# Optimization experiments

Measured on AMD Instinct MI355X. Metric: run time of the kernel, lower is better.

## Reference

```python
import jax, jax.numpy as jnp
import numpy as np
import math

B, S, H = 8, 1024, 768
NH = 12
DH = H // NH


def _linear(x, W, b):
    # torch Linear: y = x @ W.T + b, W: [out, in]
    return jnp.einsum('bsd,ed->bse', x, W) + b


def _split_heads(x):
    # [B,S,H] -> [B,NH,S,DH]
    b, s, _ = x.shape
    return x.reshape(b, s, NH, DH).transpose(0, 2, 1, 3)


def _attend(q, k, v):
    # q,k,v: [B,NH,S,DH]
    scores = jnp.einsum('bhqd,bhkd->bhqk', q, k) / math.sqrt(DH)
    probs = jax.nn.softmax(scores, axis=-1)
    ctx = jnp.einsum('bhqk,bhkd->bhqd', probs, v)
    b, h, s, d = ctx.shape
    return ctx.transpose(0, 2, 1, 3).reshape(b, s, h * d)


def setup_inputs() -> dict:
    key = jax.random.key(0)
    ks = jax.random.split(key, 20)
    sc = 1.0 / math.sqrt(H)
    inp = {
        'hidden_statesx': jax.random.normal(ks[0], (B, S, H), jnp.float32),
        'hidden_statesy': jax.random.normal(ks[1], (B, S, H), jnp.float32),
    }
    names = ['Wq', 'Wk', 'Wv', 'Wo', 'Wqd', 'Wkd', 'Wvd', 'Wod']
    for i, n in enumerate(names):
        inp[n] = jax.random.normal(ks[2 + i], (H, H), jnp.float32) * sc
        inp['b' + n[1:]] = jnp.zeros((H,), jnp.float32)
    inp['w11'] = jnp.full((1,), 0.5, jnp.float32)
    inp['w12'] = jnp.full((1,), 0.5, jnp.float32)
    inp['w21'] = jnp.full((1,), 0.5, jnp.float32)
    inp['w22'] = jnp.full((1,), 0.5, jnp.float32)
    return inp


def reference(hidden_statesx, hidden_statesy,
              Wq, bq, Wk, bk, Wv, bv, Wo, bo,
              Wqd, bqd, Wkd, bkd, Wvd, bvd, Wod, bod,
              w11, w12, w21, w22):
    q = _split_heads(_linear(hidden_statesx, Wq, bq))
    k = _split_heads(_linear(hidden_statesx, Wk, bk))
    v = _split_heads(_linear(hidden_statesx, Wv, bv))
    qd = _split_heads(_linear(hidden_statesy, Wqd, bqd))
    kd = _split_heads(_linear(hidden_statesy, Wkd, bkd))
    vd = _split_heads(_linear(hidden_statesy, Wvd, bvd))

    # self-attention on x and y streams
    attention_sx = _linear(_attend(q, k, v), Wo, bo)
    attention_sy = _linear(_attend(qd, kd, vd), Wod, bod)
    # cross attentions (mba mode)
    attention_cx = _linear(_attend(q, kd, vd), Wo, bo)
    attention_cy = _linear(_attend(qd, k, v), Wod, bod)

    attention_sx = w11 * attention_sx + w12 * attention_cx
    attention_sy = w21 * attention_sy + w22 * attention_cy
    return attention_sx, attention_sy
```

## Files before the change

kernel.cpp:

```cpp
#include <hip/hip_runtime.h>

typedef __bf16 bf16;
typedef __bf16 bf16x8 __attribute__((ext_vector_type(8)));
typedef float f32x4 __attribute__((ext_vector_type(4)));

#define HD 768
#define ELTS 6291456
#define WELTS 589824

__device__ __forceinline__ void gld_lds16(const bf16* g, bf16* l) {
  __builtin_amdgcn_global_load_lds((const __attribute__((address_space(1))) void*)g,
                                   (__attribute__((address_space(3))) void*)l, 16, 0, 0);
}

__device__ __forceinline__ float rdscalar(const void* p, int f) {
  return f ? (float)((const bf16*)p)[0] : ((const float*)p)[0];
}

__device__ __forceinline__ float exp2fast(float x) {
#if __has_builtin(__builtin_amdgcn_exp2f)
  return __builtin_amdgcn_exp2f(x);
#else
  return __builtin_exp2f(x);
#endif
}

__global__ void probe_dtype(const unsigned int* __restrict__ x, int* flag) {
  const int t = threadIdx.x;
  int bad = 0;
#pragma unroll
  for (int i = 0; i < 4; ++i) {
    unsigned int wd = x[t * 4 + i];
    unsigned int e0 = (wd >> 7) & 0xFF;
    unsigned int e1 = (wd >> 23) & 0xFF;
    bad += (e0 >= 134) + (e1 >= 134);
  }
  unsigned long long m = __ballot(bad > 0);
  if (t == 0) *flag = (m == 0ULL) ? 1 : 0;
}

struct CvtArgs {
  const float* src[20];
  bf16* dst[20];
  int n[20];
  const int* flag;
};
__global__ __launch_bounds__(256) void convert_inputs(CvtArgs a) {
  if (*a.flag) return;
  const int seg = blockIdx.y;
  const float* s = a.src[seg];
  bf16* d = a.dst[seg];
  const int n4 = a.n[seg] >> 2;
  for (int i = blockIdx.x * blockDim.x + threadIdx.x; i < n4; i += gridDim.x * blockDim.x) {
    f32x4 v = *(const f32x4*)(s + i * 4);
    bf16 o[4];
#pragma unroll
    for (int e = 0; e < 4; ++e) o[e] = (bf16)v[e];
    *(unsigned long long*)(d + i * 4) = *(unsigned long long*)o;
  }
}

struct GemmArgs {
  const void* A[6];
  const void* Ac[6];
  const void* W[6];
  const void* Wc[6];
  const void* bias[6];
  const void* biasc[6];
  const void* s0[6];
  const void* s1[6];
  void* C[6];
  float cmul[6];
  int c_fixed[6];
  int vt[6];
  int ext_w[6];
  long long out_elem_off[6];
  const int* flag;
};

__global__ __launch_bounds__(256) void gemm_bt(GemmArgs args) {
  const int g = blockIdx.z;
  const int f = *args.flag;
  const bool c_bf = args.c_fixed[g] || f;
  const bool w_f32 = (!f) && args.ext_w[g];
  const bf16* __restrict__ A = (const bf16*)(f ? args.A[g] : args.Ac[g]);
  const void* __restrict__ Wp = f ? args.W[g] : args.Wc[g];
  const void* __restrict__ bias = f ? args.bias[g] : args.biasc[g];
  bf16* Cb = (bf16*)args.C[g] + args.out_elem_off[g];
  float* Cf = (float*)args.C[g] + args.out_elem_off[g];
  float bscale = 1.0f;
  if (args.s0[g]) bscale = rdscalar(args.s0[g], f) + rdscalar(args.s1[g], f);
  const float cmul = args.cmul[g];

  const int m0 = blockIdx.x * 128;
  const int n0 = blockIdx.y * 128;
  const int t = threadIdx.x;
  const int lane = t & 63;
  const int w = t >> 6;
  const int wm = (w >> 1) * 64, wn = (w & 1) * 64;

  __shared__ __attribute__((aligned(16))) bf16 As[128 * 32];
  __shared__ __attribute__((aligned(16))) bf16 Bs[128 * 32];

  f32x4 acc[4][4] = {};

  const int c0 = t, c1 = t + 256;
  const int r0 = c0 >> 2, k40 = (c0 & 3) * 8;
  const int r1 = c1 >> 2, k41 = (c1 & 3) * 8;
  const int fr = lane & 15;
  const int fo = (lane >> 4) * 8;

  for (int kb = 0; kb < 24; ++kb) {
    const int k0 = kb * 32;
    gld_lds16(A + (size_t)(m0 + r0) * HD + k0 + k40, As + c0 * 8);
    gld_lds16(A + (size_t)(m0 + r1) * HD + k0 + k41, As + c1 * 8);
    const size_t iw0 = (size_t)(n0 + r0) * HD + k0 + k40;
    const size_t iw1 = (size_t)(n0 + r1) * HD + k0 + k41;
    if (!w_f32) {
      gld_lds16((const bf16*)Wp + iw0, Bs + c0 * 8);
      gld_lds16((const bf16*)Wp + iw1, Bs + c1 * 8);
    } else {
      const float* Wf = (const float*)Wp;
      f32x4 u0 = *(const f32x4*)(Wf + iw0), u1 = *(const f32x4*)(Wf + iw0 + 4);
      f32x4 u2 = *(const f32x4*)(Wf + iw1), u3 = *(const f32x4*)(Wf + iw1 + 4);
      bf16x8 v0, v1;
#pragma unroll
      for (int e = 0; e < 4; ++e) { v0[e] = (bf16)u0[e]; v0[e + 4] = (bf16)u1[e];
                                    v1[e] = (bf16)u2[e]; v1[e + 4] = (bf16)u3[e]; }
      *(bf16x8*)(Bs + c0 * 8) = v0;
      *(bf16x8*)(Bs + c1 * 8) = v1;
    }
    __syncthreads();
    bf16x8 af[4], bfr[4];
#pragma unroll
    for (int mi = 0; mi < 4; ++mi)
      af[mi] = *(const bf16x8*)(As + (wm + mi * 16 + fr) * 32 + fo);
#pragma unroll
    for (int ni = 0; ni < 4; ++ni)
      bfr[ni] = *(const bf16x8*)(Bs + (wn + ni * 16 + fr) * 32 + fo);
#pragma unroll
    for (int mi = 0; mi < 4; ++mi)
#pragma unroll
      for (int ni = 0; ni < 4; ++ni)
        acc[mi][ni] = __builtin_amdgcn_mfma_f32_16x16x32_bf16(af[mi], bfr[ni], acc[mi][ni], 0, 0, 0);
    __syncthreads();
  }

  const int rq = (lane >> 4) * 4;
  const int is_vt = args.vt[g];
#pragma unroll
  for (int ni = 0; ni < 4; ++ni) {
    const int col = n0 + wn + ni * 16 + fr;
    const float bv = (w_f32 ? ((const float*)bias)[col]
                            : (float)((const bf16*)bias)[col]) * bscale;
#pragma unroll
    for (int mi = 0; mi < 4; ++mi) {
      const int row = m0 + wm + mi * 16 + rq;
      if (is_vt) {
        const int bb = row >> 10, s = row & 1023;
        const int hh = col >> 6, d = col & 63;
        bf16 tmp[4];
#pragma unroll
        for (int r = 0; r < 4; ++r) tmp[r] = (bf16)((acc[mi][ni][r] + bv) * cmul);
        *(unsigned long long*)(Cb + (((size_t)(bb * 12 + hh)) << 16) + (d << 10) + s) =
            *(const unsigned long long*)tmp;
      } else {
#pragma unroll
        for (int r = 0; r < 4; ++r) {
          const float val = (acc[mi][ni][r] + bv) * cmul;
          if (c_bf) Cb[(size_t)(row + r) * HD + col] = (bf16)val;
          else      Cf[(size_t)(row + r) * HD + col] = val;
        }
      }
    }
  }
}

__global__ __launch_bounds__(256, 5) void attn_mba(
    const bf16* __restrict__ Q, const bf16* __restrict__ Kx, const bf16* __restrict__ Vtx,
    const bf16* __restrict__ Qd, const bf16* __restrict__ Kd, const bf16* __restrict__ Vtd,
    const void* w11, const void* w12, const void* w21, const void* w22,
    bf16* ctxX, bf16* ctxY, const int* flag) {
  const int linear = blockIdx.x + (blockIdx.y << 4) + blockIdx.z * 1536;
  const int swz = (linear & 7) * 384 + (linear >> 3);
  const int qb = swz & 15;
  const int bhz = swz >> 4;
  const int z = bhz >= 96 ? 1 : 0;
  const int bh = bhz - z * 96;
  const int b = bh / 12;
  const int f = *flag;

  const bf16* Qp  = z ? Qd  : Q;
  const bf16* Kc0 = z ? Kd  : Kx;
  const bf16* Vc0 = z ? Vtd : Vtx;
  const bf16* Kc1 = z ? Kx  : Kd;
  const bf16* Vc1 = z ? Vtx : Vtd;
  const float wgt0 = z ? rdscalar(w21, f) : rdscalar(w11, f);
  const float wgt1 = z ? rdscalar(w22, f) : rdscalar(w12, f);
  bf16* Out = z ? ctxY : ctxX;

  const size_t tok0 = (size_t)b * 1024;
  const size_t vbase = (size_t)bh * 65536;
  const int fcol = (bh - b * 12) * 64;
  const int q0 = qb * 64;

  __shared__ __attribute__((aligned(16))) bf16 smem[16384];
  bf16* Ks = smem;
  bf16* Vs = smem + 8192;

  const int t = threadIdx.x, lane = t & 63, w = t >> 6;
  const int l15 = lane & 15, l4 = lane >> 4;

  auto stage = [&](int nit) {
    const bf16* Kc = nit < 16 ? Kc0 : Kc1;
    const bf16* Vc = nit < 16 ? Vc0 : Vc1;
    const int kt = nit & 15;
    bf16* Kb = Ks + (nit & 1) * 4096;
    bf16* Vb = Vs + (nit & 1) * 4096;
#pragma unroll
    for (int i = 0; i < 2; ++i) {
      const int q = t + i * 256;
      const int g = q >> 3, slot = q & 7;
      const int gs = (slot ^ (g & 7)) << 3;
      const int kp = (g & 32) + ((g & 12) << 1) + ((g & 16) >> 2) + (g & 3);
      gld_lds16(Kc + (tok0 + kt * 64 + kp) * HD + fcol + gs, Kb + q * 8);
      gld_lds16(Vc + vbase + (size_t)g * 1024 + kt * 64 + gs, Vb + q * 8);
    }
  };

  stage(0);

  const int qrow = w * 16 + l15;
  const bf16* qbase = Qp + (tok0 + q0 + qrow) * HD + fcol;
  const bf16x8 qf0 = *(const bf16x8*)(qbase + (l4 << 3));
  const bf16x8 qf1 = *(const bf16x8*)(qbase + ((4 + l4) << 3));

  int koff0[4], koff1[4];
#pragma unroll
  for (int mi = 0; mi < 4; ++mi) {
    const int kr = mi * 16 + l15;
    koff0[mi] = kr * 64 + ((l4 ^ (kr & 7)) << 3);
    koff1[mi] = kr * 64 + (((4 + l4) ^ (kr & 7)) << 3);
  }

  __syncthreads();

  f32x4 mixT[4] = {};
  f32x4 oaccT[4] = {};
  float m_r = -INFINITY, l_r = 0.0f;

  for (int it = 0; it < 32; ++it) {
    if (it) __syncthreads();
    if (it + 1 < 32) stage(it + 1);
    const bf16* Kb = Ks + (it & 1) * 4096;
    const bf16* Vb = Vs + (it & 1) * 4096;

    float pv[4][4];
    float mx = -INFINITY;
    __builtin_amdgcn_s_setprio(1);
#pragma unroll
    for (int mi = 0; mi < 4; ++mi) {
      bf16x8 kf0 = *(const bf16x8*)(Kb + koff0[mi]);
      bf16x8 kf1 = *(const bf16x8*)(Kb + koff1[mi]);
      f32x4 s = {};
      s = __builtin_amdgcn_mfma_f32_16x16x32_bf16(kf0, qf0, s, 0, 0, 0);
      s = __builtin_amdgcn_mfma_f32_16x16x32_bf16(kf1, qf1, s, 0, 0, 0);
      pv[mi][0] = s[0]; pv[mi][1] = s[1]; pv[mi][2] = s[2]; pv[mi][3] = s[3];
      mx = fmaxf(fmaxf(mx, s[0]), s[1]);
      mx = fmaxf(fmaxf(mx, s[2]), s[3]);
    }
    __builtin_amdgcn_s_setprio(0);
    mx = fmaxf(mx, __shfl_xor(mx, 16));
    mx = fmaxf(mx, __shfl_xor(mx, 32));

    if (!__all(mx <= m_r + 8.0f)) {
      const float mnew = fmaxf(m_r, mx);
      const float alpha = exp2fast(m_r - mnew);
      l_r *= alpha;
#pragma unroll
      for (int mi = 0; mi < 4; ++mi) oaccT[mi] *= alpha;
      m_r = mnew;
    }

    float sum = 0.0f;
#pragma unroll
    for (int mi = 0; mi < 4; ++mi)
#pragma unroll
      for (int r = 0; r < 4; ++r) {
        pv[mi][r] = exp2fast(pv[mi][r] - m_r);
        sum += pv[mi][r];
      }
    sum += __shfl_xor(sum, 16);
    sum += __shfl_xor(sum, 32);
    l_r += sum;

#pragma unroll
    for (int c = 0; c < 2; ++c) {
      bf16x8 pf;
#pragma unroll
      for (int j = 0; j < 8; ++j)
        pf[j] = (bf16)pv[2 * c + (j >> 2)][j & 3];
      __builtin_amdgcn_s_setprio(1);
#pragma unroll
      for (int mi = 0; mi < 4; ++mi) {
        bf16x8 vf = *(const bf16x8*)(Vb + (c ? koff1[mi] : koff0[mi]));
        oaccT[mi] = __builtin_amdgcn_mfma_f32_16x16x32_bf16(vf, pf, oaccT[mi], 0, 0, 0);
      }
      __builtin_amdgcn_s_setprio(0);
    }

    if ((it & 15) == 15) {
      const float sc = (it < 16 ? wgt0 : wgt1) / l_r;
#pragma unroll
      for (int mi = 0; mi < 4; ++mi) {
#pragma unroll
        for (int r = 0; r < 4; ++r) mixT[mi][r] += sc * oaccT[mi][r];
        oaccT[mi] = f32x4{};
      }
      m_r = -INFINITY; l_r = 0.0f;
    }
  }

  __syncthreads();
  bf16* T = smem;
#pragma unroll
  for (int mi = 0; mi < 4; ++mi)
#pragma unroll
    for (int r = 0; r < 4; ++r)
      T[qrow * 72 + mi * 16 + l4 * 4 + r] = (bf16)mixT[mi][r];
  __syncthreads();
#pragma unroll
  for (int i = 0; i < 2; ++i) {
    const int q = t + i * 256;
    const int g = q >> 3, dc = (q & 7) * 8;
    *(bf16x8*)(Out + (tok0 + q0 + g) * HD + fcol + dc) = *(const bf16x8*)(T + g * 72 + dc);
  }
}

extern "C" void kernel_launch(void* const* d_in, const int* in_sizes, int n_in,
                              void* d_out, int out_size, void* d_ws, size_t ws_size,
                              hipStream_t stream) {
  (void)in_sizes; (void)n_in; (void)out_size;
  const void* x = d_in[0];
  const void* y = d_in[1];

  bf16* ws = (bf16*)d_ws;
  bf16* Qb   = ws + 0ull * ELTS;
  bf16* Kb   = ws + 1ull * ELTS;
  bf16* Vtb  = ws + 2ull * ELTS;
  bf16* Qdb  = ws + 3ull * ELTS;
  bf16* Kdb  = ws + 4ull * ELTS;
  bf16* Vtdb = ws + 5ull * ELTS;
  bf16* ctxX = Qb;
  bf16* ctxY = Qdb;
  int* flag = (int*)(ws + 6ull * ELTS);

  const size_t extra_elems = 6ull * ELTS + 32 + 2ull * WELTS + 2 * 768;
  const bool big_ws = ws_size >= extra_elems * sizeof(bf16);
  bf16* extraW = ws + 6ull * ELTS + 32;
  bf16* extraB = extraW + 2ull * WELTS;

  bf16* cb = (bf16*)d_out;
  bf16* xb = cb;
  bf16* yb = cb + (size_t)ELTS;
  bf16* Wcv = cb + 2ull * ELTS;
  bf16* bcv = Wcv + 6ull * WELTS;

  probe_dtype<<<dim3(1), dim3(64), 0, stream>>>((const unsigned int*)x, flag);

  CvtArgs ca;
  int nseg = 14;
  {
    const int wsrc[6] = {2, 4, 6, 10, 12, 14};
    ca.src[0] = (const float*)x;  ca.dst[0] = xb;  ca.n[0] = ELTS;
    ca.src[1] = (const float*)y;  ca.dst[1] = yb;  ca.n[1] = ELTS;
    for (int i = 0; i < 6; ++i) {
      ca.src[2 + i] = (const float*)d_in[wsrc[i]];
      ca.dst[2 + i] = Wcv + (size_t)i * WELTS;
      ca.n[2 + i] = WELTS;
      ca.src[8 + i] = (const float*)d_in[wsrc[i] + 1];
      ca.dst[8 + i] = bcv + (size_t)i * 768;
      ca.n[8 + i] = 768;
    }
    if (big_ws) {
      ca.src[14] = (const float*)d_in[8];  ca.dst[14] = extraW;         ca.n[14] = WELTS;
      ca.src[15] = (const float*)d_in[16]; ca.dst[15] = extraW + WELTS; ca.n[15] = WELTS;
      ca.src[16] = (const float*)d_in[9];  ca.dst[16] = extraB;         ca.n[16] = 768;
      ca.src[17] = (const float*)d_in[17]; ca.dst[17] = extraB + 768;   ca.n[17] = 768;
      nseg = 18;
    }
    ca.flag = flag;
  }
  convert_inputs<<<dim3(512, nseg), dim3(256), 0, stream>>>(ca);

  GemmArgs gq;
  {
    const void* A6[6]  = {x, x, x, y, y, y};
    const void* Ac6[6] = {xb, xb, xb, yb, yb, yb};
    const int di[6] = {2, 4, 6, 10, 12, 14};
    bf16* C6[6] = {Qb, Kb, Vtb, Qdb, Kdb, Vtdb};
    for (int i = 0; i < 6; ++i) {
      gq.A[i] = A6[i]; gq.Ac[i] = Ac6[i];
      gq.W[i] = d_in[di[i]]; gq.Wc[i] = Wcv + (size_t)i * WELTS;
      gq.bias[i] = d_in[di[i] + 1]; gq.biasc[i] = bcv + (size_t)i * 768;
      gq.s0[i] = nullptr; gq.s1[i] = nullptr; gq.C[i] = C6[i];
      gq.cmul[i] = (i == 0 || i == 3) ? 0.18033688011112042f : 1.0f;
      gq.c_fixed[i] = 1; gq.ext_w[i] = 0; gq.out_elem_off[i] = 0;
      gq.vt[i] = (i == 2 || i == 5) ? 1 : 0;
    }
    gq.flag = flag;
  }
  gemm_bt<<<dim3(64, 6, 6), dim3(256), 0, stream>>>(gq);

  attn_mba<<<dim3(16, 96, 2), dim3(256), 0, stream>>>(
      Qb, Kb, Vtb, Qdb, Kdb, Vtdb, d_in[18], d_in[19], d_in[20], d_in[21],
      ctxX, ctxY, flag);

  GemmArgs gp;
  for (int i = 0; i < 6; ++i) {
    gp.A[i] = ctxX; gp.Ac[i] = ctxX;
    gp.W[i] = d_in[8]; gp.Wc[i] = d_in[8];
    gp.bias[i] = d_in[9]; gp.biasc[i] = d_in[9];
    gp.s0[i] = d_in[18]; gp.s1[i] = d_in[19]; gp.C[i] = d_out;
    gp.cmul[i] = 1.0f; gp.c_fixed[i] = 0; gp.vt[i] = 0;
    gp.ext_w[i] = 1; gp.out_elem_off[i] = 0;
  }
  gp.A[1] = ctxY; gp.Ac[1] = ctxY;
  gp.W[1] = d_in[16]; gp.Wc[1] = d_in[16];
  gp.bias[1] = d_in[17]; gp.biasc[1] = d_in[17];
  gp.s0[1] = d_in[20]; gp.s1[1] = d_in[21];
  gp.out_elem_off[1] = (long long)ELTS;
  if (big_ws) {
    gp.Wc[0] = extraW;         gp.biasc[0] = extraB;       gp.ext_w[0] = 0;
    gp.Wc[1] = extraW + WELTS; gp.biasc[1] = extraB + 768; gp.ext_w[1] = 0;
  }
  gp.flag = flag;
  gemm_bt<<<dim3(64, 6, 2), dim3(256), 0, stream>>>(gp);
}
```

Baseline: 430.7 us.

## Share K/V tiles across both query streams and widen GEMM K-tile with swizzle

The attention kernel now processes both the x and y query streams in one block. Each staged K/V tile (Kx/Vx, then Kd/Vd) is reused for two online-softmax states, so the grid halves and global K/V traffic is cut in half. Mixing weights are remapped per stream: the y output gets w22 for the x keys and w21 for the self keys. Separately, the projection GEMM doubles its K tile to 64 with an XOR-swizzled LDS layout, which halves the barrier count and reduces bank conflicts. The costs are higher register pressure in attention (launch bounds drop to 4) and less parallelism.

```diff
diff --git a/kernel.cpp b/kernel.cpp
--- a/kernel.cpp
+++ b/kernel.cpp
@@ -99,50 +99,62 @@
   const int w = t >> 6;
   const int wm = (w >> 1) * 64, wn = (w & 1) * 64;
 
-  __shared__ __attribute__((aligned(16))) bf16 As[128 * 32];
-  __shared__ __attribute__((aligned(16))) bf16 Bs[128 * 32];
+  __shared__ __attribute__((aligned(16))) bf16 As[128 * 64];
+  __shared__ __attribute__((aligned(16))) bf16 Bs[128 * 64];
 
   f32x4 acc[4][4] = {};
 
-  const int c0 = t, c1 = t + 256;
-  const int r0 = c0 >> 2, k40 = (c0 & 3) * 8;
-  const int r1 = c1 >> 2, k41 = (c1 & 3) * 8;
+  const int row_s = t >> 3, slot_s = t & 7;
+  const int gswz = (slot_s ^ (row_s & 7)) << 3;
+
   const int fr = lane & 15;
-  const int fo = (lane >> 4) * 8;
-
-  for (int kb = 0; kb < 24; ++kb) {
-    const int k0 = kb * 32;
-    gld_lds16(A + (size_t)(m0 + r0) * HD + k0 + k40, As + c0 * 8);
-    gld_lds16(A + (size_t)(m0 + r1) * HD + k0 + k41, As + c1 * 8);
-    const size_t iw0 = (size_t)(n0 + r0) * HD + k0 + k40;
-    const size_t iw1 = (size_t)(n0 + r1) * HD + k0 + k41;
+  const int l4 = lane >> 4;
+  const int sR0 = ((l4) ^ (fr & 7)) << 3;
+  const int sR1 = ((4 + l4) ^ (fr & 7)) << 3;
+
+  for (int kb = 0; kb < 12; ++kb) {
+    const int k0 = kb * 64;
+#pragma unroll
+    for (int i = 0; i < 4; ++i) {
+      const int row = row_s + i * 32;
+      gld_lds16(A + (size_t)(m0 + row) * HD + k0 + gswz, As + (t + i * 256) * 8);
+    }
     if (!w_f32) {
-      gld_lds16((const bf16*)Wp + iw0, Bs + c0 * 8);
-      gld_lds16((const bf16*)Wp + iw1, Bs + c1 * 8);
+#pragma unroll
+      for (int i = 0; i < 4; ++i) {
+        const int row = row_s + i * 32;
+        gld_lds16((const bf16*)Wp + (size_t)(n0 + row) * HD + k0 + gswz, Bs + (t + i * 256) * 8);
+      }
     } else {
       const float* Wf = (const float*)Wp;
-      f32x4 u0 = *(const f32x4*)(Wf + iw0), u1 = *(const f32x4*)(Wf + iw0 + 4);
-      f32x4 u2 = *(const f32x4*)(Wf + iw1), u3 = *(const f32x4*)(Wf + iw1 + 4);
-      bf16x8 v0, v1;
-#pragma unroll
-      for (int e = 0; e < 4; ++e) { v0[e] = (bf16)u0[e]; v0[e + 4] = (bf16)u1[e];
-                                    v1[e] = (bf16)u2[e]; v1[e + 4] = (bf16)u3[e]; }
-      *(bf16x8*)(Bs + c0 * 8) = v0;
-      *(bf16x8*)(Bs + c1 * 8) = v1;
+#pragma unroll
+      for (int i = 0; i < 4; ++i) {
+        const int row = row_s + i * 32;
+        const size_t src = (size_t)(n0 + row) * HD + k0 + gswz;
+        f32x4 u0 = *(const f32x4*)(Wf + src), u1 = *(const f32x4*)(Wf + src + 4);
+        bf16x8 v;
+#pragma unroll
+        for (int e = 0; e < 4; ++e) { v[e] = (bf16)u0[e]; v[e + 4] = (bf16)u1[e]; }
+        *(bf16x8*)(Bs + (t + i * 256) * 8) = v;
+      }
     }
     __syncthreads();
-    bf16x8 af[4], bfr[4];
-#pragma unroll
-    for (int mi = 0; mi < 4; ++mi)
-      af[mi] = *(const bf16x8*)(As + (wm + mi * 16 + fr) * 32 + fo);
-#pragma unroll
-    for (int ni = 0; ni < 4; ++ni)
-      bfr[ni] = *(const bf16x8*)(Bs + (wn + ni * 16 + fr) * 32 + fo);
-#pragma unroll
-    for (int mi = 0; mi < 4; ++mi)
+#pragma unroll
+    for (int kk = 0; kk < 2; ++kk) {
+      const int sR = kk ? sR1 : sR0;
+      bf16x8 af[4], bfr[4];
+#pragma unroll
+      for (int mi = 0; mi < 4; ++mi)
+        af[mi] = *(const bf16x8*)(As + (wm + mi * 16 + fr) * 64 + sR);
 #pragma unroll
       for (int ni = 0; ni < 4; ++ni)
-        acc[mi][ni] = __builtin_amdgcn_mfma_f32_16x16x32_bf16(af[mi], bfr[ni], acc[mi][ni], 0, 0, 0);
+        bfr[ni] = *(const bf16x8*)(Bs + (wn + ni * 16 + fr) * 64 + sR);
+#pragma unroll
+      for (int mi = 0; mi < 4; ++mi)
+#pragma unroll
+        for (int ni = 0; ni < 4; ++ni)
+          acc[mi][ni] = __builtin_amdgcn_mfma_f32_16x16x32_bf16(af[mi], bfr[ni], acc[mi][ni], 0, 0, 0);
+    }
     __syncthreads();
   }
 
@@ -176,28 +188,20 @@
   }
 }
 
-__global__ __launch_bounds__(256, 5) void attn_mba(
+__global__ __launch_bounds__(256, 4) void attn_mba(
     const bf16* __restrict__ Q, const bf16* __restrict__ Kx, const bf16* __restrict__ Vtx,
     const bf16* __restrict__ Qd, const bf16* __restrict__ Kd, const bf16* __restrict__ Vtd,
     const void* w11, const void* w12, const void* w21, const void* w22,
     bf16* ctxX, bf16* ctxY, const int* flag) {
-  const int linear = blockIdx.x + (blockIdx.y << 4) + blockIdx.z * 1536;
-  const int swz = (linear & 7) * 384 + (linear >> 3);
+  const int linear = blockIdx.x + (blockIdx.y << 4);
+  const int swz = (linear & 7) * 192 + (linear >> 3);
   const int qb = swz & 15;
-  const int bhz = swz >> 4;
-  const int z = bhz >= 96 ? 1 : 0;
-  const int bh = bhz - z * 96;
+  const int bh = swz >> 4;
   const int b = bh / 12;
   const int f = *flag;
 
-  const bf16* Qp  = z ? Qd  : Q;
-  const bf16* Kc0 = z ? Kd  : Kx;
-  const bf16* Vc0 = z ? Vtd : Vtx;
-  const bf16* Kc1 = z ? Kx  : Kd;
-  const bf16* Vc1 = z ? Vtx : Vtd;
-  const float wgt0 = z ? rdscalar(w21, f) : rdscalar(w11, f);
-  const float wgt1 = z ? rdscalar(w22, f) : rdscalar(w12, f);
-  bf16* Out = z ? ctxY : ctxX;
+  const float wgtX[2] = {rdscalar(w11, f), rdscalar(w12, f)};
+  const float wgtY[2] = {rdscalar(w22, f), rdscalar(w21, f)};
 
   const size_t tok0 = (size_t)b * 1024;
   const size_t vbase = (size_t)bh * 65536;
@@ -212,8 +216,8 @@
   const int l15 = lane & 15, l4 = lane >> 4;
 
   auto stage = [&](int nit) {
-    const bf16* Kc = nit < 16 ? Kc0 : Kc1;
-    const bf16* Vc = nit < 16 ? Vc0 : Vc1;
+    const bf16* Kc = nit < 16 ? Kx : Kd;
+    const bf16* Vc = nit < 16 ? Vtx : Vtd;
     const int kt = nit & 15;
     bf16* Kb = Ks + (nit & 1) * 4096;
     bf16* Vb = Vs + (nit & 1) * 4096;
@@ -231,9 +235,13 @@
   stage(0);
 
   const int qrow = w * 16 + l15;
-  const bf16* qbase = Qp + (tok0 + q0 + qrow) * HD + fcol;
-  const bf16x8 qf0 = *(const bf16x8*)(qbase + (l4 << 3));
-  const bf16x8 qf1 = *(const bf16x8*)(qbase + ((4 + l4) << 3));
+  const bf16* qb0 = Q  + (tok0 + q0 + qrow) * HD + fcol;
+  const bf16* qb1 = Qd + (tok0 + q0 + qrow) * HD + fcol;
+  bf16x8 qf[2][2];
+  qf[0][0] = *(const bf16x8*)(qb0 + (l4 << 3));
+  qf[0][1] = *(const bf16x8*)(qb0 + ((4 + l4) << 3));
+  qf[1][0] = *(const bf16x8*)(qb1 + (l4 << 3));
+  qf[1][1] = *(const bf16x8*)(qb1 + ((4 + l4) << 3));
 
   int koff0[4], koff1[4];
 #pragma unroll
@@ -245,9 +253,10 @@
 
   __syncthreads();
 
-  f32x4 mixT[4] = {};
-  f32x4 oaccT[4] = {};
-  float m_r = -INFINITY, l_r = 0.0f;
+  f32x4 mixX[4] = {}, mixY[4] = {};
+  f32x4 oacc[2][4] = {};
+  float m_s[2] = {-INFINITY, -INFINITY};
+  float l_s[2] = {0.0f, 0.0f};
 
   for (int it = 0; it < 32; ++it) {
     if (it) __syncthreads();
@@ -255,85 +264,99 @@
     const bf16* Kb = Ks + (it & 1) * 4096;
     const bf16* Vb = Vs + (it & 1) * 4096;
 
-    float pv[4][4];
-    float mx = -INFINITY;
-    __builtin_amdgcn_s_setprio(1);
-#pragma unroll
-    for (int mi = 0; mi < 4; ++mi) {
-      bf16x8 kf0 = *(const bf16x8*)(Kb + koff0[mi]);
-      bf16x8 kf1 = *(const bf16x8*)(Kb + koff1[mi]);
-      f32x4 s = {};
-      s = __builtin_amdgcn_mfma_f32_16x16x32_bf16(kf0, qf0, s, 0, 0, 0);
-      s = __builtin_amdgcn_mfma_f32_16x16x32_bf16(kf1, qf1, s, 0, 0, 0);
-      pv[mi][0] = s[0]; pv[mi][1] = s[1]; pv[mi][2] = s[2]; pv[mi][3] = s[3];
-      mx = fmaxf(fmaxf(mx, s[0]), s[1]);
-      mx = fmaxf(fmaxf(mx, s[2]), s[3]);
-    }
-    __builtin_amdgcn_s_setprio(0);
-    mx = fmaxf(mx, __shfl_xor(mx, 16));
-    mx = fmaxf(mx, __shfl_xor(mx, 32));
-
-    if (!__all(mx <= m_r + 8.0f)) {
-      const float mnew = fmaxf(m_r, mx);
-      const float alpha = exp2fast(m_r - mnew);
-      l_r *= alpha;
-#pragma unroll
-      for (int mi = 0; mi < 4; ++mi) oaccT[mi] *= alpha;
-      m_r = mnew;
-    }
-
-    float sum = 0.0f;
-#pragma unroll
-    for (int mi = 0; mi < 4; ++mi)
-#pragma unroll
-      for (int r = 0; r < 4; ++r) {
-        pv[mi][r] = exp2fast(pv[mi][r] - m_r);
-        sum += pv[mi][r];
-      }
-    sum += __shfl_xor(sum, 16);
-    sum += __shfl_xor(sum, 32);
-    l_r += sum;
-
-#pragma unroll
-    for (int c = 0; c < 2; ++c) {
-      bf16x8 pf;
-#pragma unroll
-      for (int j = 0; j < 8; ++j)
-        pf[j] = (bf16)pv[2 * c + (j >> 2)][j & 3];
+#pragma unroll
+    for (int s2 = 0; s2 < 2; ++s2) {
+      float pv[4][4];
+      float mx = -INFINITY;
       __builtin_amdgcn_s_setprio(1);
 #pragma unroll
       for (int mi = 0; mi < 4; ++mi) {
-        bf16x8 vf = *(const bf16x8*)(Vb + (c ? koff1[mi] : koff0[mi]));
-        oaccT[mi] = __builtin_amdgcn_mfma_f32_16x16x32_bf16(vf, pf, oaccT[mi], 0, 0, 0);
+        bf16x8 kf0 = *(const bf16x8*)(Kb + koff0[mi]);
+        bf16x8 kf1 = *(const bf16x8*)(Kb + koff1[mi]);
+        f32x4 s = {};
+        s = __builtin_amdgcn_mfma_f32_16x16x32_bf16(kf0, qf[s2][0], s, 0, 0, 0);
+        s = __builtin_amdgcn_mfma_f32_16x16x32_bf16(kf1, qf[s2][1], s, 0, 0, 0);
+        pv[mi][0] = s[0]; pv[mi][1] = s[1]; pv[mi][2] = s[2]; pv[mi][3] = s[3];
+        mx = fmaxf(fmaxf(mx, s[0]), s[1]);
+        mx = fmaxf(fmaxf(mx, s[2]), s[3]);
       }
       __builtin_amdgcn_s_setprio(0);
+      mx = fmaxf(mx, __shfl_xor(mx, 16));
+      mx = fmaxf(mx, __shfl_xor(mx, 32));
+
+      if (!__all(mx <= m_s[s2] + 8.0f)) {
+        const float mnew = fmaxf(m_s[s2], mx);
+        const float alpha = exp2fast(m_s[s2] - mnew);
+        l_s[s2] *= alpha;
+#pragma unroll
+        for (int mi = 0; mi < 4; ++mi) oacc[s2][mi] *= alpha;
+        m_s[s2] = mnew;
+      }
+
+      float sum = 0.0f;
+#pragma unroll
+      for (int mi = 0; mi < 4; ++mi)
+#pragma unroll
+        for (int r = 0; r < 4; ++r) {
+          pv[mi][r] = exp2fast(pv[mi][r] - m_s[s2]);
+          sum += pv[mi][r];
+        }
+      sum += __shfl_xor(sum, 16);
+      sum += __shfl_xor(sum, 32);
+      l_s[s2] += sum;
+
+#pragma unroll
+      for (int c = 0; c < 2; ++c) {
+        bf16x8 pf;
+#pragma unroll
+        for (int j = 0; j < 8; ++j)
+          pf[j] = (bf16)pv[2 * c + (j >> 2)][j & 3];
+        __builtin_amdgcn_s_setprio(1);
+#pragma unroll
+        for (int mi = 0; mi < 4; ++mi) {
+          bf16x8 vf = *(const bf16x8*)(Vb + (c ? koff1[mi] : koff0[mi]));
+          oacc[s2][mi] = __builtin_amdgcn_mfma_f32_16x16x32_bf16(vf, pf, oacc[s2][mi], 0, 0, 0);
+        }
+        __builtin_amdgcn_s_setprio(0);
+      }
     }
 
     if ((it & 15) == 15) {
-      const float sc = (it < 16 ? wgt0 : wgt1) / l_r;
+      const int ph = it >> 4;
+      const float scX = wgtX[ph] / l_s[0];
+      const float scY = wgtY[ph] / l_s[1];
 #pragma unroll
       for (int mi = 0; mi < 4; ++mi) {
 #pragma unroll
-        for (int r = 0; r < 4; ++r) mixT[mi][r] += sc * oaccT[mi][r];
-        oaccT[mi] = f32x4{};
-      }
-      m_r = -INFINITY; l_r = 0.0f;
+        for (int r = 0; r < 4; ++r) {
+          mixX[mi][r] += scX * oacc[0][mi][r];
+          mixY[mi][r] += scY * oacc[1][mi][r];
+        }
+        oacc[0][mi] = f32x4{};
+        oacc[1][mi] = f32x4{};
+      }
+      m_s[0] = m_s[1] = -INFINITY;
+      l_s[0] = l_s[1] = 0.0f;
     }
   }
 
   __syncthreads();
-  bf16* T = smem;
+  bf16* TX = smem;
+  bf16* TY = smem + 4608;
 #pragma unroll
   for (int mi = 0; mi < 4; ++mi)
 #pragma unroll
-    for (int r = 0; r < 4; ++r)
-      T[qrow * 72 + mi * 16 + l4 * 4 + r] = (bf16)mixT[mi][r];
+    for (int r = 0; r < 4; ++r) {
+      TX[qrow * 72 + mi * 16 + l4 * 4 + r] = (bf16)mixX[mi][r];
+      TY[qrow * 72 + mi * 16 + l4 * 4 + r] = (bf16)mixY[mi][r];
+    }
   __syncthreads();
 #pragma unroll
   for (int i = 0; i < 2; ++i) {
     const int q = t + i * 256;
     const int g = q >> 3, dc = (q & 7) * 8;
-    *(bf16x8*)(Out + (tok0 + q0 + g) * HD + fcol + dc) = *(const bf16x8*)(T + g * 72 + dc);
+    *(bf16x8*)(ctxX + (tok0 + q0 + g) * HD + fcol + dc) = *(const bf16x8*)(TX + g * 72 + dc);
+    *(bf16x8*)(ctxY + (tok0 + q0 + g) * HD + fcol + dc) = *(const bf16x8*)(TY + g * 72 + dc);
   }
 }
 
@@ -412,7 +435,7 @@
   }
   gemm_bt<<<dim3(64, 6, 6), dim3(256), 0, stream>>>(gq);
 
-  attn_mba<<<dim3(16, 96, 2), dim3(256), 0, stream>>>(
+  attn_mba<<<dim3(16, 96), dim3(256), 0, stream>>>(
       Qb, Kb, Vtb, Qdb, Kdb, Vtdb, d_in[18], d_in[19], d_in[20], d_in[21],
       ctxX, ctxY, flag);
 
```

New measurement: 415.1 us. 3.6% less time.
